# Kernel optimization log

Hardware: AMD Instinct MI355X
Metric: run time of the kernel (lower is better)

The kernel has to match this reference:

```python
import jax, jax.numpy as jnp
import numpy as np
import math

B, S, H, NH = 2, 2048, 1024, 16
DH = H // NH  # 64
REL_VOCAB = 4096  # 2 * (max_position_embeddings // 4)


def setup_inputs() -> dict:
    key = jax.random.key(0)
    ks = jax.random.split(key, 9)
    s = 0.02
    return {
        "hidden_states": jax.random.normal(ks[0], (B, S, H), jnp.float32),
        "attention_mask": jnp.zeros((B, 1, 1, S), jnp.float32),
        "distance_idx": jax.random.randint(ks[1], (S, S), 0, REL_VOCAB),
        "Wq": jax.random.normal(ks[2], (H, H), jnp.float32) * s,
        "bq": jnp.zeros((H,), jnp.float32),
        "Wk": jax.random.normal(ks[3], (H, H), jnp.float32) * s,
        "bk": jnp.zeros((H,), jnp.float32),
        "Wv": jax.random.normal(ks[4], (H, H), jnp.float32) * s,
        "bv": jnp.zeros((H,), jnp.float32),
        "dist_emb": jax.random.normal(ks[5], (REL_VOCAB, NH), jnp.float32) * s,
    }


def _heads(x):
    # [B,S,H] -> [B,NH,S,DH]
    return x.reshape(B, S, NH, DH).transpose(0, 2, 1, 3)


def reference(hidden_states, attention_mask, distance_idx, Wq, bq, Wk, bk, Wv, bv, dist_emb):
    q = _heads(hidden_states @ Wq.T + bq)
    k = _heads(hidden_states @ Wk.T + bk)
    v = _heads(hidden_states @ Wv.T + bv)
    # scores: [B,NH,S,S]
    scores = jnp.einsum("bhqd,bhkd->bhqk", q, k) / math.sqrt(DH)
    # relative_scalar_bias: embed(distance_idx) [S,S,NH] -> [1,NH,S,S]
    bias = dist_emb[distance_idx].transpose(2, 0, 1)[None]
    scores = scores + bias  # attention_scores_terms == 1 -> /sqrt(1)
    scores = scores + attention_mask
    probs = jax.nn.softmax(scores, axis=-1)
    ctx = jnp.einsum("bhqk,bhkd->bhqd", probs, v)
    return ctx.transpose(0, 2, 1, 3).reshape(B, S, H)
```

## Files before the change

### kernel.cpp

```cpp
#include <hip/hip_runtime.h>
#include <hip/hip_bf16.h>

#define B_   2
#define S_   2048
#define H_   1024
#define NH_  16
#define DH_  64

typedef __attribute__((ext_vector_type(8))) __bf16 bf16x8;
typedef __attribute__((ext_vector_type(8))) unsigned short u16x8;
typedef __attribute__((ext_vector_type(4))) float f32x4;

typedef const __attribute__((address_space(1))) unsigned int gu32_t;
typedef __attribute__((address_space(3))) unsigned int su32_t;

static __device__ inline unsigned short f2bf(float x) {
    union { float f; unsigned u; } v; v.f = x;
    unsigned r = v.u + 0x7fffu + ((v.u >> 16) & 1u);
    return (unsigned short)(r >> 16);
}

static __device__ inline unsigned short f2bf_r(float x) {
    union { float f; unsigned u; } v; v.f = x;
    return (unsigned short)((v.u + 0x8000u) >> 16);
}

static __device__ inline float bf2f(unsigned short u) {
    union { unsigned u; float f; } v; v.u = ((unsigned)u) << 16;
    return v.f;
}

static __device__ inline bf16x8 ldfrag(const unsigned short* p) {
    return __builtin_bit_cast(bf16x8, *(const u16x8*)p);
}

__global__ void conv_all(const float* __restrict__ x,
                         const float* __restrict__ Wq, const float* __restrict__ Wk,
                         const float* __restrict__ Wv, const float* __restrict__ demb,
                         unsigned short* __restrict__ xb, unsigned short* __restrict__ wall,
                         unsigned short* __restrict__ dembT) {
    int bid = blockIdx.x, tid = threadIdx.x;
    if (bid < 4096) {
        int i = bid * 256 + tid;
        float4 v = ((const float4*)x)[i];
        ushort4 o;
        o.x = f2bf(v.x); o.y = f2bf(v.y); o.z = f2bf(v.z); o.w = f2bf(v.w);
        ((ushort4*)xb)[i] = o;
    } else if (bid < 7168) {
        int i = (bid - 4096) * 256 + tid;
        int e = i * 4;
        int which = e >> 20;
        int r4 = (e & ((1 << 20) - 1)) >> 2;
        const float* src = which == 0 ? Wq : which == 1 ? Wk : Wv;
        float4 v = ((const float4*)src)[r4];
        ushort4 o;
        o.x = f2bf(v.x); o.y = f2bf(v.y); o.z = f2bf(v.z); o.w = f2bf(v.w);
        ((ushort4*)wall)[i] = o;
    } else {
        int t = (bid - 7168) * 256 + tid;
        int h = t >> 12, e = t & 4095;
        dembT[t] = f2bf(demb[e * 16 + h]);
    }
}

__global__ __launch_bounds__(256) void gemm_qkv(
    const unsigned short* __restrict__ Xb, const unsigned short* __restrict__ Wall,
    const float* __restrict__ bq, const float* __restrict__ bk, const float* __restrict__ bv,
    unsigned short* __restrict__ Q, unsigned short* __restrict__ K, unsigned short* __restrict__ V)
{
    __shared__ unsigned short As[128 * 32];
    __shared__ unsigned short Bs[128 * 32];
    const int tid = threadIdx.x, lane = tid & 63, wv = tid >> 6;
    const int g = lane >> 4, l16 = lane & 15;
    const int wm = wv >> 1, wn = wv & 1;
    const int bm = blockIdx.y, bn = blockIdx.x;

    const int lrow = lane >> 2, lcol = (lane & 3) * 8;

    f32x4 acc[4][4];
    #pragma unroll
    for (int i = 0; i < 4; ++i)
        #pragma unroll
        for (int j = 0; j < 4; ++j) acc[i][j] = (f32x4){0.f, 0.f, 0.f, 0.f};

    for (int kt = 0; kt < 32; ++kt) {
        #pragma unroll
        for (int i = 0; i < 2; ++i) {
            int chunk = wv * 2 + i;
            int row = chunk * 16 + lrow;
            const unsigned short* ga = &Xb[(size_t)(bm * 128 + row) * 1024 + kt * 32 + lcol];
            const unsigned short* gb = &Wall[(size_t)(bn * 128 + row) * 1024 + kt * 32 + lcol];
            __builtin_amdgcn_global_load_lds((gu32_t*)(const void*)ga, (su32_t*)(void*)&As[chunk * 512], 16, 0, 0);
            __builtin_amdgcn_global_load_lds((gu32_t*)(const void*)gb, (su32_t*)(void*)&Bs[chunk * 512], 16, 0, 0);
        }
        __syncthreads();
        bf16x8 a[4], b[4];
        #pragma unroll
        for (int mi = 0; mi < 4; ++mi) a[mi] = ldfrag(&As[(wm * 64 + mi * 16 + l16) * 32 + g * 8]);
        #pragma unroll
        for (int ni = 0; ni < 4; ++ni) b[ni] = ldfrag(&Bs[(wn * 64 + ni * 16 + l16) * 32 + g * 8]);
        #pragma unroll
        for (int mi = 0; mi < 4; ++mi)
            #pragma unroll
            for (int ni = 0; ni < 4; ++ni)
                acc[mi][ni] = __builtin_amdgcn_mfma_f32_16x16x32_bf16(a[mi], b[ni], acc[mi][ni], 0, 0, 0);
        __syncthreads();
    }

    #pragma unroll
    for (int mi = 0; mi < 4; ++mi) {
        #pragma unroll
        for (int ni = 0; ni < 4; ++ni) {
            int gn = bn * 128 + wn * 64 + ni * 16 + l16;
            int which = gn >> 10, nn = gn & 1023;
            int h = nn >> 6, d = nn & 63;
            float bias = which == 0 ? bq[nn] : which == 1 ? bk[nn] : bv[nn];
            unsigned short* dst = which == 0 ? Q : which == 1 ? K : V;
            #pragma unroll
            for (int r = 0; r < 4; ++r) {
                int gm = bm * 128 + wm * 64 + mi * 16 + g * 4 + r;
                int bb = gm >> 11, s = gm & 2047;
                dst[((size_t)(bb * 16 + h) * 2048 + s) * 64 + d] = f2bf(acc[mi][ni][r] + bias);
            }
        }
    }
}

__global__ void transpose_v(const unsigned short* __restrict__ V, unsigned short* __restrict__ VT) {
    __shared__ unsigned short t[64][65];
    int bh = blockIdx.y, st = blockIdx.x, tid = threadIdx.x;
    size_t ib = (size_t)bh * S_ * DH_ + (size_t)st * 64 * 64;
    #pragma unroll
    for (int rep = 0; rep < 16; ++rep) {
        int e = rep * 256 + tid;
        t[e >> 6][e & 63] = V[ib + e];
    }
    __syncthreads();
    size_t ob = (size_t)bh * DH_ * S_ + st * 64;
    #pragma unroll
    for (int rep = 0; rep < 16; ++rep) {
        int e = rep * 256 + tid;
        int d = e >> 6, sl = e & 63;
        VT[ob + (size_t)d * S_ + sl] = t[sl][d];
    }
}

__global__ __launch_bounds__(256, 4) void attn(
    const unsigned short* __restrict__ Q, const unsigned short* __restrict__ K,
    const unsigned short* __restrict__ VT, const int* __restrict__ didx,
    const unsigned short* __restrict__ dembT, const float* __restrict__ mask,
    float* __restrict__ out)
{
    __shared__ unsigned short demb_h[4096];
    __shared__ unsigned short Ks[64 * 64];
    __shared__ unsigned short Vs[64 * 64];
    __shared__ unsigned short Ps[4][16 * 64];
    const int tid = threadIdx.x, lane = tid & 63, w = tid >> 6;
    const int g = lane >> 4, l16 = lane & 15;
    const int h = blockIdx.x, qt = blockIdx.y, b = blockIdx.z;
    const int bh = b * NH_ + h;
    const int qr = qt * 64 + w * 16;

    #pragma unroll
    for (int j = 0; j < 2; ++j) {
        int i = j * 256 + tid;
        *(uint4*)&demb_h[i * 8] = *(const uint4*)&dembT[h * 4096 + i * 8];
    }

    bf16x8 qf[2];
    {
        size_t qbase = ((size_t)bh * S_ + qr + l16) * DH_;
        qf[0] = ldfrag(&Q[qbase + g * 8]);
        qf[1] = ldfrag(&Q[qbase + 32 + g * 8]);
    }

    f32x4 oa[4];
    float lsum[4];
    #pragma unroll
    for (int i = 0; i < 4; ++i) {
        oa[i] = (f32x4){0.f, 0.f, 0.f, 0.f};
        lsum[i] = 0.f;
    }

    const size_t kbase = (size_t)bh * S_ * DH_;
    const size_t vbase = (size_t)bh * DH_ * S_;

    __syncthreads();

    for (int kt = 0; kt < 32; ++kt) {
        #pragma unroll
        for (int j = 0; j < 2; ++j) {
            int e = j * 2048 + tid * 8;
            int r = e >> 6, c = e & 63;
            int sidx = r * 64 + ((((c >> 3) ^ (r & 7))) << 3);
            *(uint4*)&Ks[sidx] = *(const uint4*)&K[kbase + (size_t)kt * 64 * 64 + e];
            *(uint4*)&Vs[sidx] = *(const uint4*)&VT[vbase + (size_t)r * S_ + kt * 64 + c];
        }

        int ei[4][4];
        float mk[4];
        #pragma unroll
        for (int kj = 0; kj < 4; ++kj) {
            int kg = kt * 64 + kj * 16 + l16;
            mk[kj] = mask[b * S_ + kg];
            #pragma unroll
            for (int r = 0; r < 4; ++r) {
                int qg = qr + g * 4 + r;
                ei[kj][r] = didx[qg * S_ + kg];
            }
        }

        __syncthreads();

        f32x4 sc[4];
        #pragma unroll
        for (int kj = 0; kj < 4; ++kj) {
            int row = kj * 16 + l16, m = row & 7;
            bf16x8 kf0 = ldfrag(&Ks[row * 64 + ((g ^ m) << 3)]);
            bf16x8 kf1 = ldfrag(&Ks[row * 64 + (((g + 4) ^ m) << 3)]);
            f32x4 z = (f32x4){0.f, 0.f, 0.f, 0.f};
            z = __builtin_amdgcn_mfma_f32_16x16x32_bf16(qf[0], kf0, z, 0, 0, 0);
            z = __builtin_amdgcn_mfma_f32_16x16x32_bf16(qf[1], kf1, z, 0, 0, 0);
            sc[kj] = z;
        }

        #pragma unroll
        for (int kj = 0; kj < 4; ++kj) {
            #pragma unroll
            for (int r = 0; r < 4; ++r) {
                float bm = bf2f(demb_h[ei[kj][r]]) + mk[kj];
                float p = __expf(fmaf(sc[kj][r], 0.125f, bm));
                lsum[r] += p;
                int row = g * 4 + r;
                int idx = row * 64 + ((((kj * 2 + (l16 >> 3)) ^ (row & 7))) << 3) + (l16 & 7);
                Ps[w][idx] = f2bf_r(p);
            }
        }

        int pm = l16 & 7;
        bf16x8 pf0 = ldfrag(&Ps[w][l16 * 64 + ((g ^ pm) << 3)]);
        bf16x8 pf1 = ldfrag(&Ps[w][l16 * 64 + (((g + 4) ^ pm) << 3)]);
        #pragma unroll
        for (int dt = 0; dt < 4; ++dt) {
            int row = dt * 16 + l16, m = row & 7;
            bf16x8 vf0 = ldfrag(&Vs[row * 64 + ((g ^ m) << 3)]);
            bf16x8 vf1 = ldfrag(&Vs[row * 64 + (((g + 4) ^ m) << 3)]);
            oa[dt] = __builtin_amdgcn_mfma_f32_16x16x32_bf16(pf0, vf0, oa[dt], 0, 0, 0);
            oa[dt] = __builtin_amdgcn_mfma_f32_16x16x32_bf16(pf1, vf1, oa[dt], 0, 0, 0);
        }
        __syncthreads();
    }

    float linv[4];
    #pragma unroll
    for (int r = 0; r < 4; ++r) {
        float s = lsum[r];
        s += __shfl_xor(s, 1);
        s += __shfl_xor(s, 2);
        s += __shfl_xor(s, 4);
        s += __shfl_xor(s, 8);
        linv[r] = __builtin_amdgcn_rcpf(s);
    }

    #pragma unroll
    for (int dt = 0; dt < 4; ++dt) {
        #pragma unroll
        for (int r = 0; r < 4; ++r) {
            int s = qr + g * 4 + r;
            int d = dt * 16 + l16;
            out[((size_t)b * S_ + s) * H_ + h * DH_ + d] = oa[dt][r] * linv[r];
        }
    }
}

extern "C" void kernel_launch(void* const* d_in, const int* in_sizes, int n_in,
                              void* d_out, int out_size, void* d_ws, size_t ws_size,
                              hipStream_t stream) {
    const float* hidden = (const float*)d_in[0];
    const float* mask   = (const float*)d_in[1];
    const int*   didx   = (const int*)d_in[2];
    const float* Wq     = (const float*)d_in[3];
    const float* bq     = (const float*)d_in[4];
    const float* Wk     = (const float*)d_in[5];
    const float* bk     = (const float*)d_in[6];
    const float* Wv     = (const float*)d_in[7];
    const float* bv     = (const float*)d_in[8];
    const float* demb   = (const float*)d_in[9];
    float* out = (float*)d_out;

    unsigned short* ws = (unsigned short*)d_ws;
    unsigned short* Xb   = ws;
    unsigned short* Wall = Xb + 4096 * 1024;
    unsigned short* Qb   = Wall + 3072 * 1024;
    unsigned short* Kb   = Qb + 4194304;
    unsigned short* Vb   = Kb + 4194304;
    unsigned short* VTb  = Vb + 4194304;
    unsigned short* DembT = VTb + 4194304;

    conv_all<<<7424, 256, 0, stream>>>(hidden, Wq, Wk, Wv, demb, Xb, Wall, DembT);
    gemm_qkv<<<dim3(24, 32), 256, 0, stream>>>(Xb, Wall, bq, bk, bv, Qb, Kb, Vb);
    transpose_v<<<dim3(32, 32), 256, 0, stream>>>(Vb, VTb);
    attn<<<dim3(16, 32, 2), 256, 0, stream>>>(Qb, Kb, VTb, didx, DembT, mask, out);
}
```

Baseline: 221.4 us.

## Compute transposed QK scores so P feeds PV MFMA from registers

```diff
diff --git a/kernel.cpp b/kernel.cpp
--- a/kernel.cpp
+++ b/kernel.cpp
@@ -10,6 +10,7 @@
 typedef __attribute__((ext_vector_type(8))) __bf16 bf16x8;
 typedef __attribute__((ext_vector_type(8))) unsigned short u16x8;
 typedef __attribute__((ext_vector_type(4))) float f32x4;
+typedef __attribute__((ext_vector_type(4))) short i16x4;
 
 typedef const __attribute__((address_space(1))) unsigned int gu32_t;
 typedef __attribute__((address_space(3))) unsigned int su32_t;
@@ -33,6 +34,12 @@
 static __device__ inline bf16x8 ldfrag(const unsigned short* p) {
     return __builtin_bit_cast(bf16x8, *(const u16x8*)p);
 }
+
+#if __has_builtin(__builtin_amdgcn_mfma_f32_16x16x16bf16_1k)
+#define MFMA16(a, b, c) __builtin_amdgcn_mfma_f32_16x16x16bf16_1k((a), (b), (c), 0, 0, 0)
+#else
+#define MFMA16(a, b, c) (c)
+#endif
 
 __global__ void conv_all(const float* __restrict__ x,
                          const float* __restrict__ Wq, const float* __restrict__ Wk,
@@ -154,7 +161,6 @@
     __shared__ unsigned short demb_h[4096];
     __shared__ unsigned short Ks[64 * 64];
     __shared__ unsigned short Vs[64 * 64];
-    __shared__ unsigned short Ps[4][16 * 64];
     const int tid = threadIdx.x, lane = tid & 63, w = tid >> 6;
     const int g = lane >> 4, l16 = lane & 15;
     const int h = blockIdx.x, qt = blockIdx.y, b = blockIdx.z;
@@ -175,15 +181,13 @@
     }
 
     f32x4 oa[4];
-    float lsum[4];
-    #pragma unroll
-    for (int i = 0; i < 4; ++i) {
-        oa[i] = (f32x4){0.f, 0.f, 0.f, 0.f};
-        lsum[i] = 0.f;
-    }
+    #pragma unroll
+    for (int i = 0; i < 4; ++i) oa[i] = (f32x4){0.f, 0.f, 0.f, 0.f};
+    float lsum = 0.f;
 
     const size_t kbase = (size_t)bh * S_ * DH_;
     const size_t vbase = (size_t)bh * DH_ * S_;
+    const int qg = qr + l16;
 
     __syncthreads();
 
@@ -193,23 +197,18 @@
             int e = j * 2048 + tid * 8;
             int r = e >> 6, c = e & 63;
             int sidx = r * 64 + ((((c >> 3) ^ (r & 7))) << 3);
-            *(uint4*)&Ks[sidx] = *(const uint4*)&K[kbase + (size_t)kt * 64 * 64 + e];
+            *(uint4*)&Ks[sidx] = *(const uint4*)&K[kbase + (size_t)kt * 4096 + e];
             *(uint4*)&Vs[sidx] = *(const uint4*)&VT[vbase + (size_t)r * S_ + kt * 64 + c];
         }
 
-        int ei[4][4];
-        float mk[4];
-        #pragma unroll
-        for (int kj = 0; kj < 4; ++kj) {
-            int kg = kt * 64 + kj * 16 + l16;
-            mk[kj] = mask[b * S_ + kg];
-            #pragma unroll
-            for (int r = 0; r < 4; ++r) {
-                int qg = qr + g * 4 + r;
-                ei[kj][r] = didx[qg * S_ + kg];
-            }
-        }
-
+        int4   di[4];
+        float4 mv[4];
+        #pragma unroll
+        for (int kj = 0; kj < 4; ++kj) {
+            int kg = kt * 64 + kj * 16 + g * 4;
+            di[kj] = *(const int4*)&didx[qg * S_ + kg];
+            mv[kj] = *(const float4*)&mask[b * S_ + kg];
+        }
         __syncthreads();
 
         f32x4 sc[4];
@@ -219,48 +218,44 @@
             bf16x8 kf0 = ldfrag(&Ks[row * 64 + ((g ^ m) << 3)]);
             bf16x8 kf1 = ldfrag(&Ks[row * 64 + (((g + 4) ^ m) << 3)]);
             f32x4 z = (f32x4){0.f, 0.f, 0.f, 0.f};
-            z = __builtin_amdgcn_mfma_f32_16x16x32_bf16(qf[0], kf0, z, 0, 0, 0);
-            z = __builtin_amdgcn_mfma_f32_16x16x32_bf16(qf[1], kf1, z, 0, 0, 0);
-            sc[kj] = z;
+            z = __builtin_amdgcn_mfma_f32_16x16x32_bf16(kf0, qf[0], z, 0, 0, 0);
+            sc[kj] = __builtin_amdgcn_mfma_f32_16x16x32_bf16(kf1, qf[1], z, 0, 0, 0);
+        }
+
+        i16x4 pa[4];
+        #pragma unroll
+        for (int kj = 0; kj < 4; ++kj) {
+            float p0 = __expf(fmaf(sc[kj][0], 0.125f, bf2f(demb_h[di[kj].x]) + mv[kj].x));
+            float p1 = __expf(fmaf(sc[kj][1], 0.125f, bf2f(demb_h[di[kj].y]) + mv[kj].y));
+            float p2 = __expf(fmaf(sc[kj][2], 0.125f, bf2f(demb_h[di[kj].z]) + mv[kj].z));
+            float p3 = __expf(fmaf(sc[kj][3], 0.125f, bf2f(demb_h[di[kj].w]) + mv[kj].w));
+            lsum += (p0 + p1) + (p2 + p3);
+            pa[kj][0] = (short)f2bf_r(p0);
+            pa[kj][1] = (short)f2bf_r(p1);
+            pa[kj][2] = (short)f2bf_r(p2);
+            pa[kj][3] = (short)f2bf_r(p3);
         }
 
         #pragma unroll
         for (int kj = 0; kj < 4; ++kj) {
             #pragma unroll
-            for (int r = 0; r < 4; ++r) {
-                float bm = bf2f(demb_h[ei[kj][r]]) + mk[kj];
-                float p = __expf(fmaf(sc[kj][r], 0.125f, bm));
-                lsum[r] += p;
-                int row = g * 4 + r;
-                int idx = row * 64 + ((((kj * 2 + (l16 >> 3)) ^ (row & 7))) << 3) + (l16 & 7);
-                Ps[w][idx] = f2bf_r(p);
+            for (int dt = 0; dt < 4; ++dt) {
+                int vrow = dt * 16 + l16, vm = vrow & 7;
+                int chunkc = kj * 2 + (g >> 1);
+                int addr = vrow * 64 + (((chunkc ^ vm)) << 3) + ((g & 1) << 2);
+                i16x4 vf = *(const i16x4*)&Vs[addr];
+                oa[dt] = MFMA16(pa[kj], vf, oa[dt]);
             }
         }
-
-        int pm = l16 & 7;
-        bf16x8 pf0 = ldfrag(&Ps[w][l16 * 64 + ((g ^ pm) << 3)]);
-        bf16x8 pf1 = ldfrag(&Ps[w][l16 * 64 + (((g + 4) ^ pm) << 3)]);
-        #pragma unroll
-        for (int dt = 0; dt < 4; ++dt) {
-            int row = dt * 16 + l16, m = row & 7;
-            bf16x8 vf0 = ldfrag(&Vs[row * 64 + ((g ^ m) << 3)]);
-            bf16x8 vf1 = ldfrag(&Vs[row * 64 + (((g + 4) ^ m) << 3)]);
-            oa[dt] = __builtin_amdgcn_mfma_f32_16x16x32_bf16(pf0, vf0, oa[dt], 0, 0, 0);
-            oa[dt] = __builtin_amdgcn_mfma_f32_16x16x32_bf16(pf1, vf1, oa[dt], 0, 0, 0);
-        }
-        __syncthreads();
-    }
-
+        __syncthreads();
+    }
+
+    lsum += __shfl_xor(lsum, 16);
+    lsum += __shfl_xor(lsum, 32);
     float linv[4];
     #pragma unroll
-    for (int r = 0; r < 4; ++r) {
-        float s = lsum[r];
-        s += __shfl_xor(s, 1);
-        s += __shfl_xor(s, 2);
-        s += __shfl_xor(s, 4);
-        s += __shfl_xor(s, 8);
-        linv[r] = __builtin_amdgcn_rcpf(s);
-    }
+    for (int r = 0; r < 4; ++r)
+        linv[r] = __builtin_amdgcn_rcpf(__shfl(lsum, g * 4 + r));
 
     #pragma unroll
     for (int dt = 0; dt < 4; ++dt) {
```

Result: slower. 238.7 us (+7.8%).
